# Performance work log

Hardware: AMD Instinct MI355X
Metric: run time of the kernel (lower is better)

Reference implementation:

```python
import jax, jax.numpy as jnp
import numpy as np

B, M, D, H, F, N = 8, 1024, 1024, 16, 4096, 4
DK = D // H
EPS = 1e-5


def _ln(x, g, b):
    mu = jnp.mean(x, axis=-1, keepdims=True)
    var = jnp.mean(jnp.square(x - mu), axis=-1, keepdims=True)
    return (x - mu) * jax.lax.rsqrt(var + EPS) * g + b


def setup_inputs() -> dict:
    key = jax.random.key(0)
    ks = jax.random.split(key, 12)
    s = 0.02
    return {
        "embeds": jax.random.normal(ks[0], (B, M, D), dtype=jnp.float32),
        "weights": jax.random.normal(ks[1], (B, M), dtype=jnp.float32) * 0.1,
        "Wq": jax.random.normal(ks[2], (N, D, D), dtype=jnp.float32) * s,
        "bq": jnp.zeros((N, D), dtype=jnp.float32),
        "Wk": jax.random.normal(ks[3], (N, D, D), dtype=jnp.float32) * s,
        "bk": jnp.zeros((N, D), dtype=jnp.float32),
        "Wv": jax.random.normal(ks[4], (N, D, D), dtype=jnp.float32) * s,
        "bv": jnp.zeros((N, D), dtype=jnp.float32),
        "Wo": jax.random.normal(ks[5], (N, D, D), dtype=jnp.float32) * s,
        "bo": jnp.zeros((N, D), dtype=jnp.float32),
        "W1": jax.random.normal(ks[6], (N, D, F), dtype=jnp.float32) * s,
        "b1": jnp.zeros((N, F), dtype=jnp.float32),
        "W2": jax.random.normal(ks[7], (N, F, D), dtype=jnp.float32) * s,
        "b2": jnp.zeros((N, D), dtype=jnp.float32),
        "g1": jnp.ones((N, D), dtype=jnp.float32),
        "be1": jnp.zeros((N, D), dtype=jnp.float32),
        "g2": jnp.ones((N, D), dtype=jnp.float32),
        "be2": jnp.zeros((N, D), dtype=jnp.float32),
    }


def reference(embeds, weights, Wq, bq, Wk, bk, Wv, bv, Wo, bo,
              W1, b1, W2, b2, g1, be1, g2, be2):
    scale = 1.0 / np.sqrt(DK).astype(np.float32)
    bias = weights[:, None, None, :]  # b,1,1,m additive bias over keys

    def layer(x, p):
        wq, bq_, wk, bk_, wv, bv_, wo, bo_, w1, b1_, w2, b2_, g1_, be1_, g2_, be2_ = p
        q = (x @ wq + bq_).reshape(B, M, H, DK)
        k = (x @ wk + bk_).reshape(B, M, H, DK)
        v = (x @ wv + bv_).reshape(B, M, H, DK)
        scores = jnp.einsum("bqhd,bkhd->bhqk", q, k) * scale + bias
        attn = jax.nn.softmax(scores, axis=-1)
        o = jnp.einsum("bhqk,bkhd->bqhd", attn, v).reshape(B, M, D)
        o = o @ wo + bo_
        x = _ln(x + o, g1_, be1_)
        y = jax.nn.gelu(x @ w1 + b1_, approximate=False) @ w2 + b2_
        x = _ln(x + y, g2_, be2_)
        return x, None

    params = (Wq, bq, Wk, bk, Wv, bv, Wo, bo, W1, b1, W2, b2, g1, be1, g2, be2)
    out, _ = jax.lax.scan(layer, embeds, params)
    return out
```

## Files before the change

kernel.cpp:

```cpp
#include <hip/hip_runtime.h>
#include <hip/hip_bf16.h>

#define BB  8
#define MM  1024
#define DD  1024
#define HH  16
#define FF  4096
#define NL  4
#define DKK 64

typedef __bf16 bf16_t;
typedef __bf16 bf16x8 __attribute__((ext_vector_type(8)));
typedef __bf16 bf16x4 __attribute__((ext_vector_type(4)));
typedef float  f32x4  __attribute__((ext_vector_type(4)));

__device__ __forceinline__ void gld16(const bf16_t* g, bf16_t* l) {
    __builtin_amdgcn_global_load_lds((const __attribute__((address_space(1))) void*)g,
                                     (__attribute__((address_space(3))) void*)l,
                                     16, 0, 0);
}

__global__ __launch_bounds__(256) void cvt_x(const float* __restrict__ e,
                                             float* __restrict__ x,
                                             bf16_t* __restrict__ xb) {
    size_t i = ((size_t)blockIdx.x * 256 + threadIdx.x) * 4;
    float4 v = *(const float4*)(e + i);
    *(float4*)(x + i) = v;
    bf16x4 o;
    o[0] = (bf16_t)v.x; o[1] = (bf16_t)v.y; o[2] = (bf16_t)v.z; o[3] = (bf16_t)v.w;
    *(bf16x4*)(xb + i) = o;
}

__global__ __launch_bounds__(256) void transpose_all(const float* __restrict__ Wq,
                                                     const float* __restrict__ Wk,
                                                     const float* __restrict__ Wv,
                                                     const float* __restrict__ Wo,
                                                     const float* __restrict__ W1,
                                                     const float* __restrict__ W2,
                                                     bf16_t* __restrict__ qkvT,
                                                     bf16_t* __restrict__ WoT,
                                                     bf16_t* __restrict__ W1T,
                                                     bf16_t* __restrict__ W2T) {
    __shared__ float tile[32][33];
    const int bx = blockIdx.x;
    const float* in;
    bf16_t* out;
    int C, t;
    if (bx < 4096) {
        const int mat = bx >> 10;
        t = bx & 1023;
        C = 1024;
        in  = mat == 0 ? Wq : mat == 1 ? Wk : mat == 2 ? Wv : Wo;
        out = mat < 3 ? qkvT + (size_t)mat * DD * DD : WoT;
    } else if (bx < 8192) {
        t = bx - 4096; C = 4096; in = W1; out = W1T;
    } else {
        t = bx - 8192; C = 1024; in = W2; out = W2T;
    }
    const int cb = C >> 5;
    const int c0 = (t % cb) * 32, r0 = (t / cb) * 32;
    const int R = (C == 1024) ? ((bx < 8192) ? 1024 : 4096) : 1024;
    const int tx = threadIdx.x & 31, ty = threadIdx.x >> 5;
    for (int i = 0; i < 4; i++)
        tile[ty + i * 8][tx] = in[(size_t)(r0 + ty + i * 8) * C + c0 + tx];
    __syncthreads();
    for (int i = 0; i < 4; i++)
        out[(size_t)(c0 + ty + i * 8) * R + r0 + tx] = (bf16_t)tile[tx][ty + i * 8];
}

__global__ __launch_bounds__(256) void concat_bias(const float* __restrict__ bq,
                                                   const float* __restrict__ bk,
                                                   const float* __restrict__ bv,
                                                   float* __restrict__ out) {
    const int seg = blockIdx.x, l = blockIdx.y, t = threadIdx.x;
    const float* src = seg == 0 ? bq : seg == 1 ? bk : bv;
    float4 v = *(const float4*)(src + (size_t)l * 1024 + t * 4);
    *(float4*)(out + (size_t)l * 3072 + seg * 1024 + t * 4) = v;
}

__global__ __launch_bounds__(256) void transpose_v_k(const bf16_t* __restrict__ v,
                                                     bf16_t* __restrict__ vT, int ld) {
    __shared__ bf16_t t[64][65];
    int bh = blockIdx.y, b = bh >> 4, h = bh & 15;
    int m0 = blockIdx.x * 64;
    int tx = threadIdx.x & 63, ty = threadIdx.x >> 6;
    for (int i = 0; i < 16; i++) {
        int mr = ty * 16 + i;
        t[mr][tx] = v[(size_t)(b * MM + m0 + mr) * ld + h * DKK + tx];
    }
    __syncthreads();
    for (int i = 0; i < 16; i++) {
        int dk = ty * 16 + i;
        vT[((size_t)(bh * DKK + dk)) * MM + m0 + tx] = t[tx][dk];
    }
}

template <int EPI>
__global__ __launch_bounds__(256) void gemm_bt(const bf16_t* __restrict__ A,
                                               const bf16_t* __restrict__ Bt,
                                               const float* __restrict__ bias,
                                               const float* __restrict__ res,
                                               bf16_t* __restrict__ outb,
                                               float* __restrict__ outf,
                                               int K, int Ntot) {
    __shared__ bf16_t As[128 * 32];
    __shared__ bf16_t Bs[128 * 32];
    const int tid = threadIdx.x, wave = tid >> 6, lane = tid & 63;
    const int fr = lane & 15, quad = lane >> 4;
    const int fk = quad * 8;
    const size_t bm = (size_t)blockIdx.y * 128, bn = (size_t)blockIdx.x * 128;
    const int wr = (wave >> 1) * 64, wc = (wave & 1) * 64;

    f32x4 acc[4][4] = {};

    const int sr = wave * 32 + (lane >> 2);
    const int sc = (lane & 3) * 8;
    const bf16_t* Ag = A + (bm + sr) * (size_t)K + sc;
    const bf16_t* Bg = Bt + (bn + sr) * (size_t)K + sc;
    bf16_t* Asw = &As[wave * 1024];
    bf16_t* Bsw = &Bs[wave * 1024];

    for (int k0 = 0; k0 < K; k0 += 32) {
        __syncthreads();
        gld16(Ag + k0, Asw);
        gld16(Ag + (size_t)16 * K + k0, Asw + 512);
        gld16(Bg + k0, Bsw);
        gld16(Bg + (size_t)16 * K + k0, Bsw + 512);
        __syncthreads();
        bf16x8 af[4], bfr[4];
#pragma unroll
        for (int i = 0; i < 4; i++)
            af[i] = *(const bf16x8*)&As[(wr + i * 16 + fr) * 32 + fk];
#pragma unroll
        for (int i = 0; i < 4; i++)
            bfr[i] = *(const bf16x8*)&Bs[(wc + i * 16 + fr) * 32 + fk];
#pragma unroll
        for (int mi = 0; mi < 4; mi++)
#pragma unroll
            for (int ni = 0; ni < 4; ni++)
                acc[mi][ni] = __builtin_amdgcn_mfma_f32_16x16x32_bf16(
                    af[mi], bfr[ni], acc[mi][ni], 0, 0, 0);
    }

#pragma unroll
    for (int ni = 0; ni < 4; ni++) {
        const size_t c = bn + wc + ni * 16 + fr;
        const float bv = bias[c];
#pragma unroll
        for (int mi = 0; mi < 4; mi++) {
            const size_t rbase = bm + wr + mi * 16 + quad * 4;
#pragma unroll
            for (int r = 0; r < 4; r++) {
                const size_t idx = (rbase + r) * (size_t)Ntot + c;
                float v = acc[mi][ni][r] + bv;
                if constexpr (EPI == 0) {
                    outb[idx] = (bf16_t)v;
                } else if constexpr (EPI == 1) {
                    outf[idx] = v + res[idx];
                } else {
                    float g = 0.5f * v * (1.0f + erff(v * 0.70710678118654752f));
                    outb[idx] = (bf16_t)g;
                }
            }
        }
    }
}

__global__ __launch_bounds__(256) void flash_attn(const bf16_t* __restrict__ q,
                                                  const bf16_t* __restrict__ kmat,
                                                  const bf16_t* __restrict__ vT,
                                                  const float* __restrict__ wts,
                                                  bf16_t* __restrict__ ao, int ldq) {
    __shared__ bf16_t Ks[128 * 72];
    __shared__ bf16_t Vs[64 * 136];
    bf16_t* Ps = Ks;

    const int tid = threadIdx.x;
    const int wave = tid >> 6, lane = tid & 63;
    const int fr = lane & 15, quad = lane >> 4;
    const int fk = quad * 8;
    const int bh = blockIdx.y, b = bh >> 4, h = bh & 15;
    const int q0 = blockIdx.x * 64;

    const size_t qrow = (size_t)(b * MM + q0 + wave * 16 + fr) * ldq + h * DKK;
    const bf16x8 aq0 = *(const bf16x8*)(q + qrow + fk);
    const bf16x8 aq1 = *(const bf16x8*)(q + qrow + 32 + fk);

    f32x4 oacc[4] = {};
    float lrow[4] = {0.f, 0.f, 0.f, 0.f};

    for (int kt = 0; kt < MM; kt += 128) {
        __syncthreads();
#pragma unroll
        for (int rr = 0; rr < 4; rr++) {
            const int key = rr * 32 + (tid >> 3);
            const int dkc = (tid & 7) * 8;
            *(bf16x8*)(&Ks[key * 72 + dkc]) =
                *(const bf16x8*)(kmat + (size_t)(b * MM + kt + key) * ldq + h * DKK + dkc);
            const int dkr = rr * 16 + (tid >> 4);
            const int kc = (tid & 15) * 8;
            *(bf16x8*)(&Vs[dkr * 136 + kc]) =
                *(const bf16x8*)(vT + (size_t)(bh * DKK + dkr) * MM + kt + kc);
        }
        __syncthreads();

        f32x4 s[8];
#pragma unroll
        for (int ni = 0; ni < 8; ni++) {
            const bf16_t* kp = &Ks[(ni * 16 + fr) * 72];
            f32x4 z = {0.f, 0.f, 0.f, 0.f};
            z = __builtin_amdgcn_mfma_f32_16x16x32_bf16(aq0, *(const bf16x8*)(kp + fk), z, 0, 0, 0);
            z = __builtin_amdgcn_mfma_f32_16x16x32_bf16(aq1, *(const bf16x8*)(kp + 32 + fk), z, 0, 0, 0);
            const float wv = wts[b * MM + kt + ni * 16 + fr];
#pragma unroll
            for (int r = 0; r < 4; r++) s[ni][r] = __expf(z[r] * 0.125f + wv);
        }

        float rs[4] = {0.f, 0.f, 0.f, 0.f};
#pragma unroll
        for (int ni = 0; ni < 8; ni++)
#pragma unroll
            for (int r = 0; r < 4; r++) rs[r] += s[ni][r];
#pragma unroll
        for (int off = 1; off < 16; off <<= 1)
#pragma unroll
            for (int r = 0; r < 4; r++) rs[r] += __shfl_xor(rs[r], off, 16);
#pragma unroll
        for (int r = 0; r < 4; r++) lrow[r] += rs[r];

        __syncthreads();

#pragma unroll
        for (int ni = 0; ni < 8; ni++)
#pragma unroll
            for (int r = 0; r < 4; r++)
                Ps[(wave * 16 + quad * 4 + r) * 136 + ni * 16 + fr] = (bf16_t)s[ni][r];

#pragma unroll
        for (int c2 = 0; c2 < 4; c2++) {
            const bf16x8 ap = *(const bf16x8*)(&Ps[(wave * 16 + fr) * 136 + c2 * 32 + fk]);
#pragma unroll
            for (int ni = 0; ni < 4; ni++) {
                const bf16x8 bv = *(const bf16x8*)(&Vs[(ni * 16 + fr) * 136 + c2 * 32 + fk]);
                oacc[ni] = __builtin_amdgcn_mfma_f32_16x16x32_bf16(ap, bv, oacc[ni], 0, 0, 0);
            }
        }
    }

    const size_t orow = (size_t)(b * MM + q0 + wave * 16 + quad * 4);
#pragma unroll
    for (int ni = 0; ni < 4; ni++)
#pragma unroll
        for (int r = 0; r < 4; r++) {
            const float ov = oacc[ni][r] / lrow[r];
            ao[(orow + r) * DD + h * DKK + ni * 16 + fr] = (bf16_t)ov;
        }
}

__global__ __launch_bounds__(256) void ln_k(const float* __restrict__ in,
                                            const float* __restrict__ g,
                                            const float* __restrict__ be,
                                            float* __restrict__ xout,
                                            bf16_t* __restrict__ xb) {
    const int row = blockIdx.x, t = threadIdx.x;
    const float* rp = in + (size_t)row * DD;
    float4 v = *(const float4*)(rp + t * 4);
    float s = v.x + v.y + v.z + v.w;
    float ss = v.x * v.x + v.y * v.y + v.z * v.z + v.w * v.w;
    for (int off = 1; off < 64; off <<= 1) {
        s += __shfl_xor(s, off);
        ss += __shfl_xor(ss, off);
    }
    __shared__ float sb[4], ssb[4];
    if ((t & 63) == 0) { sb[t >> 6] = s; ssb[t >> 6] = ss; }
    __syncthreads();
    s = sb[0] + sb[1] + sb[2] + sb[3];
    ss = ssb[0] + ssb[1] + ssb[2] + ssb[3];
    const float mu = s * (1.0f / DD);
    const float var = ss * (1.0f / DD) - mu * mu;
    const float rstd = rsqrtf(var + 1e-5f);
    float4 gg = *(const float4*)(g + t * 4);
    float4 bb = *(const float4*)(be + t * 4);
    float o0 = (v.x - mu) * rstd * gg.x + bb.x;
    float o1 = (v.y - mu) * rstd * gg.y + bb.y;
    float o2 = (v.z - mu) * rstd * gg.z + bb.z;
    float o3 = (v.w - mu) * rstd * gg.w + bb.w;
    *(float4*)(xout + (size_t)row * DD + t * 4) = make_float4(o0, o1, o2, o3);
    bf16x4 ob;
    ob[0] = (bf16_t)o0; ob[1] = (bf16_t)o1; ob[2] = (bf16_t)o2; ob[3] = (bf16_t)o3;
    *(bf16x4*)(xb + (size_t)row * DD + t * 4) = ob;
}

extern "C" void kernel_launch(void* const* d_in, const int* in_sizes, int n_in,
                              void* d_out, int out_size, void* d_ws, size_t ws_size,
                              hipStream_t stream) {
    const float* embeds = (const float*)d_in[0];
    const float* wts    = (const float*)d_in[1];
    const float* Wq = (const float*)d_in[2];
    const float* bq = (const float*)d_in[3];
    const float* Wk = (const float*)d_in[4];
    const float* bk = (const float*)d_in[5];
    const float* Wv = (const float*)d_in[6];
    const float* bv = (const float*)d_in[7];
    const float* Wo = (const float*)d_in[8];
    const float* bo = (const float*)d_in[9];
    const float* W1 = (const float*)d_in[10];
    const float* b1 = (const float*)d_in[11];
    const float* W2 = (const float*)d_in[12];
    const float* b2 = (const float*)d_in[13];
    const float* g1 = (const float*)d_in[14];
    const float* be1 = (const float*)d_in[15];
    const float* g2 = (const float*)d_in[16];
    const float* be2 = (const float*)d_in[17];
    float* x = (float*)d_out;

    char* p = (char*)d_ws;
    auto take = [&](size_t n) { char* r = p; p += (n + 255) & ~(size_t)255; return r; };
    const size_t nBMD = (size_t)BB * MM * DD;
    bf16_t* xb   = (bf16_t*)take(nBMD * 2);
    bf16_t* qkvb = (bf16_t*)take(nBMD * 3 * 2);
    bf16_t* vTb  = (bf16_t*)take(nBMD * 2);
    float*  r1   = (float*)take(nBMD * 4);
    float*  x1   = (float*)take(nBMD * 4);
    bf16_t* hb   = (bf16_t*)take((size_t)BB * MM * FF * 2);
    bf16_t* qkvT = (bf16_t*)take((size_t)3 * DD * DD * 2);
    bf16_t* WoT  = (bf16_t*)take((size_t)DD * DD * 2);
    bf16_t* W1T  = (bf16_t*)take((size_t)DD * FF * 2);
    bf16_t* W2T  = (bf16_t*)take((size_t)DD * FF * 2);
    float*  qkvB = (float*)take((size_t)NL * 3072 * 4);
    bf16_t* aob  = hb;
    bf16_t* x1b  = xb;

    cvt_x<<<8192, 256, 0, stream>>>(embeds, x, xb);
    concat_bias<<<dim3(3, NL), 256, 0, stream>>>(bq, bk, bv, qkvB);

    const dim3 gemmQKV(3072 / 128, (BB * MM) / 128);
    const dim3 gemmDD(DD / 128, (BB * MM) / 128);
    const dim3 gemmF1(FF / 128, (BB * MM) / 128);

    for (int l = 0; l < NL; l++) {
        transpose_all<<<12288, 256, 0, stream>>>(
            Wq + (size_t)l * DD * DD, Wk + (size_t)l * DD * DD,
            Wv + (size_t)l * DD * DD, Wo + (size_t)l * DD * DD,
            W1 + (size_t)l * DD * FF, W2 + (size_t)l * FF * DD,
            qkvT, WoT, W1T, W2T);

        gemm_bt<0><<<gemmQKV, 256, 0, stream>>>(xb, qkvT, qkvB + (size_t)l * 3072,
                                                nullptr, qkvb, nullptr, DD, 3072);

        transpose_v_k<<<dim3(16, 128), 256, 0, stream>>>(qkvb + 2048, vTb, 3072);
        flash_attn<<<dim3(16, 128), 256, 0, stream>>>(qkvb, qkvb + 1024, vTb, wts, aob, 3072);

        gemm_bt<1><<<gemmDD, 256, 0, stream>>>(aob, WoT, bo + (size_t)l * DD, x, nullptr, r1, DD, DD);
        ln_k<<<BB * MM, 256, 0, stream>>>(r1, g1 + (size_t)l * DD, be1 + (size_t)l * DD, x1, x1b);

        gemm_bt<2><<<gemmF1, 256, 0, stream>>>(x1b, W1T, b1 + (size_t)l * FF, nullptr, hb, nullptr, DD, FF);
        gemm_bt<1><<<gemmDD, 256, 0, stream>>>(hb, W2T, b2 + (size_t)l * DD, x1, nullptr, r1, FF, DD);
        ln_k<<<BB * MM, 256, 0, stream>>>(r1, g2 + (size_t)l * DD, be2 + (size_t)l * DD, x, xb);
    }
}
```

Before: 2.215 ms.

## Split-K the N=1024 projection GEMMs and fuse partial sum into layernorm

Adds a split-K GEMM variant that divides the reduction dimension in two across blockIdx.z, doubling the block count for the Wo and W2 GEMMs, which otherwise launch only 512 tiles. The first slice adds bias and residual, the second writes a raw partial into the reused qkv buffer, and the layernorm kernel now sums both inputs before normalizing. This aims to fill more compute units on the narrow output GEMMs, at the cost of an extra fp32 partial write and read per element. The new GEMM also drops whatever pipelining the original gemm_bt had, using a simple synchronous load loop.

```diff
diff --git a/kernel.cpp b/kernel.cpp
--- a/kernel.cpp
+++ b/kernel.cpp
@@ -166,6 +166,72 @@
     }
 }
 
+__global__ __launch_bounds__(256) void gemm_bt_sk(const bf16_t* __restrict__ A,
+                                                  const bf16_t* __restrict__ Bt,
+                                                  const float* __restrict__ bias,
+                                                  const float* __restrict__ res,
+                                                  float* __restrict__ outf0,
+                                                  float* __restrict__ outf1,
+                                                  int K, int Khalf, int Ntot) {
+    __shared__ bf16_t As[128 * 32];
+    __shared__ bf16_t Bs[128 * 32];
+    const int tid = threadIdx.x, wave = tid >> 6, lane = tid & 63;
+    const int fr = lane & 15, quad = lane >> 4;
+    const int fk = quad * 8;
+    const size_t bm = (size_t)blockIdx.y * 128, bn = (size_t)blockIdx.x * 128;
+    const int wr = (wave >> 1) * 64, wc = (wave & 1) * 64;
+    const int z = blockIdx.z;
+
+    f32x4 acc[4][4] = {};
+
+    const int sr = wave * 32 + (lane >> 2);
+    const int sc = (lane & 3) * 8;
+    const bf16_t* Ag = A + (size_t)z * Khalf + (bm + sr) * (size_t)K + sc;
+    const bf16_t* Bg = Bt + (size_t)z * Khalf + (bn + sr) * (size_t)K + sc;
+    bf16_t* Asw = &As[wave * 1024];
+    bf16_t* Bsw = &Bs[wave * 1024];
+
+    for (int k0 = 0; k0 < Khalf; k0 += 32) {
+        __syncthreads();
+        gld16(Ag + k0, Asw);
+        gld16(Ag + (size_t)16 * K + k0, Asw + 512);
+        gld16(Bg + k0, Bsw);
+        gld16(Bg + (size_t)16 * K + k0, Bsw + 512);
+        __syncthreads();
+        bf16x8 af[4], bfr[4];
+#pragma unroll
+        for (int i = 0; i < 4; i++)
+            af[i] = *(const bf16x8*)&As[(wr + i * 16 + fr) * 32 + fk];
+#pragma unroll
+        for (int i = 0; i < 4; i++)
+            bfr[i] = *(const bf16x8*)&Bs[(wc + i * 16 + fr) * 32 + fk];
+#pragma unroll
+        for (int mi = 0; mi < 4; mi++)
+#pragma unroll
+            for (int ni = 0; ni < 4; ni++)
+                acc[mi][ni] = __builtin_amdgcn_mfma_f32_16x16x32_bf16(
+                    af[mi], bfr[ni], acc[mi][ni], 0, 0, 0);
+    }
+
+#pragma unroll
+    for (int ni = 0; ni < 4; ni++) {
+        const size_t c = bn + wc + ni * 16 + fr;
+        const float bv = bias[c];
+#pragma unroll
+        for (int mi = 0; mi < 4; mi++) {
+            const size_t rbase = bm + wr + mi * 16 + quad * 4;
+#pragma unroll
+            for (int r = 0; r < 4; r++) {
+                const size_t idx = (rbase + r) * (size_t)Ntot + c;
+                if (z == 0)
+                    outf0[idx] = acc[mi][ni][r] + bv + res[idx];
+                else
+                    outf1[idx] = acc[mi][ni][r];
+            }
+        }
+    }
+}
+
 __global__ __launch_bounds__(256) void flash_attn(const bf16_t* __restrict__ q,
                                                   const bf16_t* __restrict__ kmat,
                                                   const bf16_t* __restrict__ vT,
@@ -257,14 +323,16 @@
         }
 }
 
-__global__ __launch_bounds__(256) void ln_k(const float* __restrict__ in,
-                                            const float* __restrict__ g,
-                                            const float* __restrict__ be,
-                                            float* __restrict__ xout,
-                                            bf16_t* __restrict__ xb) {
+__global__ __launch_bounds__(256) void ln2_k(const float* __restrict__ in0,
+                                             const float* __restrict__ in1,
+                                             const float* __restrict__ g,
+                                             const float* __restrict__ be,
+                                             float* __restrict__ xout,
+                                             bf16_t* __restrict__ xb) {
     const int row = blockIdx.x, t = threadIdx.x;
-    const float* rp = in + (size_t)row * DD;
-    float4 v = *(const float4*)(rp + t * 4);
+    float4 v  = *(const float4*)(in0 + (size_t)row * DD + t * 4);
+    float4 v1 = *(const float4*)(in1 + (size_t)row * DD + t * 4);
+    v.x += v1.x; v.y += v1.y; v.z += v1.z; v.w += v1.w;
     float s = v.x + v.y + v.z + v.w;
     float ss = v.x * v.x + v.y * v.y + v.z * v.z + v.w * v.w;
     for (int off = 1; off < 64; off <<= 1) {
@@ -330,12 +398,13 @@
     float*  qkvB = (float*)take((size_t)NL * 3072 * 4);
     bf16_t* aob  = hb;
     bf16_t* x1b  = xb;
+    float*  r1b  = (float*)qkvb;
 
     cvt_x<<<8192, 256, 0, stream>>>(embeds, x, xb);
     concat_bias<<<dim3(3, NL), 256, 0, stream>>>(bq, bk, bv, qkvB);
 
     const dim3 gemmQKV(3072 / 128, (BB * MM) / 128);
-    const dim3 gemmDD(DD / 128, (BB * MM) / 128);
+    const dim3 gemmSK(DD / 128, (BB * MM) / 128, 2);
     const dim3 gemmF1(FF / 128, (BB * MM) / 128);
 
     for (int l = 0; l < NL; l++) {
@@ -351,11 +420,14 @@
         transpose_v_k<<<dim3(16, 128), 256, 0, stream>>>(qkvb + 2048, vTb, 3072);
         flash_attn<<<dim3(16, 128), 256, 0, stream>>>(qkvb, qkvb + 1024, vTb, wts, aob, 3072);
 
-        gemm_bt<1><<<gemmDD, 256, 0, stream>>>(aob, WoT, bo + (size_t)l * DD, x, nullptr, r1, DD, DD);
-        ln_k<<<BB * MM, 256, 0, stream>>>(r1, g1 + (size_t)l * DD, be1 + (size_t)l * DD, x1, x1b);
+        gemm_bt_sk<<<gemmSK, 256, 0, stream>>>(aob, WoT, bo + (size_t)l * DD, x,
+                                               r1, r1b, DD, DD / 2, DD);
+        ln2_k<<<BB * MM, 256, 0, stream>>>(r1, r1b, g1 + (size_t)l * DD, be1 + (size_t)l * DD, x1, x1b);
 
         gemm_bt<2><<<gemmF1, 256, 0, stream>>>(x1b, W1T, b1 + (size_t)l * FF, nullptr, hb, nullptr, DD, FF);
-        gemm_bt<1><<<gemmDD, 256, 0, stream>>>(hb, W2T, b2 + (size_t)l * DD, x1, nullptr, r1, FF, DD);
-        ln_k<<<BB * MM, 256, 0, stream>>>(r1, g2 + (size_t)l * DD, be2 + (size_t)l * DD, x, xb);
-    }
-}
+
+        gemm_bt_sk<<<gemmSK, 256, 0, stream>>>(hb, W2T, b2 + (size_t)l * DD, x1,
+                                               r1, r1b, FF, FF / 2, DD);
+        ln2_k<<<BB * MM, 256, 0, stream>>>(r1, r1b, g2 + (size_t)l * DD, be2 + (size_t)l * DD, x, xb);
+    }
+}
```

After: 2.428 ms. 9.6% more time.
